# Kernel tuning notes

Hardware: AMD Instinct MI355X
Metric: run time of the kernel (lower is better)

Reference implementation:

```python
import jax, jax.numpy as jnp
import numpy as np

N_NODES = 50000
N_HEDGES = 5000
NNZ = 800000
IN_C = 128
D1 = 256
D2 = D1 // 4  # 64


def setup_inputs() -> dict:
    key = jax.random.key(0)
    ks = jax.random.split(key, 7)
    x = jax.random.normal(ks[0], (N_NODES, IN_C), dtype=jnp.float32)
    node_idx = jax.random.randint(ks[1], (NNZ,), 0, N_NODES, dtype=jnp.int32)
    hedge_idx = jax.random.randint(ks[2], (NNZ,), 0, N_HEDGES, dtype=jnp.int32)
    edge = jnp.stack([node_idx, hedge_idx], axis=0)  # [2, nnz]
    W1 = jax.random.normal(ks[3], (IN_C, D1), dtype=jnp.float32) / np.float32(np.sqrt(IN_C))
    b1 = jnp.zeros((D1,), dtype=jnp.float32)
    W2 = jax.random.normal(ks[4], (D1, D2), dtype=jnp.float32) / np.float32(np.sqrt(D1))
    b2 = jnp.zeros((D2,), dtype=jnp.float32)
    return {"x": x, "edge": edge, "W1": W1, "b1": b1, "W2": W2, "b2": b2}


def _hconv(x, W, b, node_idx, hedge_idx):
    # HypergraphConv (no attention, unit hyperedge weights):
    # out = D^{-1} H B^{-1} H^T (X W) + b
    xw = x @ W  # [N, F]
    ones = jnp.ones((node_idx.shape[0],), dtype=xw.dtype)
    deg = jax.ops.segment_sum(ones, node_idx, num_segments=N_NODES)      # D_i
    Dinv = jnp.where(deg > 0, 1.0 / deg, 0.0)
    cnt = jax.ops.segment_sum(ones, hedge_idx, num_segments=N_HEDGES)    # B_e
    Binv = jnp.where(cnt > 0, 1.0 / cnt, 0.0)
    # node -> hyperedge aggregation (gather + segment_sum), normalized by B^{-1}
    e = jax.ops.segment_sum(xw[node_idx], hedge_idx, num_segments=N_HEDGES) * Binv[:, None]
    # hyperedge -> node aggregation, normalized by D^{-1}
    out = jax.ops.segment_sum(e[hedge_idx], node_idx, num_segments=N_NODES) * Dinv[:, None]
    return out + b


def reference(x, edge, W1, b1, W2, b2):
    node_idx, hedge_idx = edge[0], edge[1]
    h = jax.nn.relu(_hconv(x, W1, b1, node_idx, hedge_idx))
    out = jax.nn.relu(_hconv(h, W2, b2, node_idx, hedge_idx))
    return out
```

## Files before the change

### kernel.cpp

```cpp
#include <hip/hip_runtime.h>

#define N_NODES 50000
#define N_HEDGES 5000
#define NNZ 800000
#define IN_C 128
#define D1 256
#define D2 64
#define SN 64
#define SH 256

#define HBK 20
#define NHB 250
#define HCAP 4096
#define NBK 100
#define NNB 500
#define NCAP 2048
#define BKT_BLOCKS ((NNZ + 2047) / 2048)

typedef unsigned int u32;
typedef unsigned short u16;
typedef __attribute__((ext_vector_type(8))) short short8;
typedef __attribute__((ext_vector_type(4))) float f32x4;

__device__ __forceinline__ float bf_lo(u32 u) { return __uint_as_float(u << 16); }
__device__ __forceinline__ float bf_hi(u32 u) { return __uint_as_float(u & 0xffff0000u); }
__device__ __forceinline__ u32 rne16(float f) {
    u32 u = __float_as_uint(f);
    return (u + 0x7fffu + ((u >> 16) & 1u)) >> 16;
}
__device__ __forceinline__ u32 pack2(float a, float b) {
    return rne16(a) | (rne16(b) << 16);
}
__device__ __forceinline__ void acc8(float* a, uint4 v) {
    a[0] += bf_lo(v.x); a[1] += bf_hi(v.x);
    a[2] += bf_lo(v.y); a[3] += bf_hi(v.y);
    a[4] += bf_lo(v.z); a[5] += bf_hi(v.z);
    a[6] += bf_lo(v.w); a[7] += bf_hi(v.w);
}

__global__ void cast_bucket(const float4* __restrict__ x, uint2* __restrict__ xb,
                            const float* __restrict__ W1, u16* __restrict__ w1hi,
                            u16* __restrict__ w1lo,
                            const float* __restrict__ W2, u16* __restrict__ w2hi,
                            u16* __restrict__ w2lo,
                            const int* __restrict__ nidx, const int* __restrict__ hidx,
                            int* __restrict__ gcur_h, int* __restrict__ gcur_n,
                            u32* __restrict__ pairs_h, u32* __restrict__ pairs_n) {
    __shared__ int hist_h[NHB], hist_n[NNB];
    __shared__ int base_h[NHB], base_n[NNB];
    int tid = threadIdx.x;
    int i = blockIdx.x * 256 + tid;
    float4 v = x[i];
    uint2 o;
    o.x = pack2(v.x, v.y);
    o.y = pack2(v.z, v.w);
    xb[i] = o;
    if (i < 32768) {
        int j = i & 7;
        int l = (i >> 3) & 63;
        int ct = (i >> 9) & 15;
        int kc = i >> 13;
        int k = kc * 32 + (l >> 4) * 8 + j;
        int n = ct * 16 + (l & 15);
        float w = W1[k * D1 + n];
        u32 h = rne16(w);
        w1hi[i] = (u16)h;
        w1lo[i] = (u16)rne16(w - bf_lo(h));
    } else if (i < 32768 + 16384) {
        int t = i - 32768;
        int j = t & 7;
        int l = (t >> 3) & 63;
        int nt = (t >> 9) & 3;
        int kc = t >> 11;
        int k = kc * 32 + (l >> 4) * 8 + j;
        int n = nt * 16 + (l & 15);
        float w = W2[k * D2 + n];
        u32 h = rne16(w);
        w2hi[t] = (u16)h;
        w2lo[t] = (u16)rne16(w - bf_lo(h));
    }
    if (blockIdx.x >= BKT_BLOCKS) return;
    for (int t = tid; t < NHB; t += 256) hist_h[t] = 0;
    for (int t = tid; t < NNB; t += 256) hist_n[t] = 0;
    __syncthreads();
    int e0 = blockIdx.x * 2048 + tid * 8;
    int ns[8], hs_[8];
#pragma unroll
    for (int k = 0; k < 8; k++) {
        int e = e0 + k;
        if (e < NNZ) {
            ns[k] = nidx[e];
            hs_[k] = hidx[e];
            atomicAdd(&hist_h[hs_[k] / HBK], 1);
            atomicAdd(&hist_n[ns[k] / NBK], 1);
        } else {
            ns[k] = -1;
        }
    }
    __syncthreads();
    if (tid < NHB) base_h[tid] = atomicAdd(&gcur_h[tid], hist_h[tid]);
    for (int t = tid; t < NNB; t += 256) base_n[t] = atomicAdd(&gcur_n[t], hist_n[t]);
    __syncthreads();
    for (int t = tid; t < NHB; t += 256) hist_h[t] = 0;
    for (int t = tid; t < NNB; t += 256) hist_n[t] = 0;
    __syncthreads();
#pragma unroll
    for (int k = 0; k < 8; k++) {
        if (ns[k] >= 0) {
            int n = ns[k], h = hs_[k];
            int bh = h / HBK, bn = n / NBK;
            int s1 = base_h[bh] + atomicAdd(&hist_h[bh], 1);
            if (s1 < HCAP) pairs_h[bh * HCAP + s1] = ((u32)h << 16) | (u32)n;
            int s2 = base_n[bn] + atomicAdd(&hist_n[bn], 1);
            if (s2 < NCAP) pairs_n[bn * NCAP + s2] = ((u32)n << 16) | (u32)h;
        }
    }
}

__global__ void build_adj(const u32* __restrict__ pairs_h, const int* __restrict__ gcur_h,
                          u16* __restrict__ adj_h, int* __restrict__ cur_h,
                          const u32* __restrict__ pairs_n, const int* __restrict__ gcur_n,
                          u16* __restrict__ adj_n, int* __restrict__ cur_n) {
    __shared__ u16 rows[NBK * SN];
    __shared__ int cnt[NBK];
    int tid = threadIdx.x;
    if (blockIdx.x < NHB) {
        int b = blockIdx.x;
        if (tid < HBK) cnt[tid] = 0;
        __syncthreads();
        int np = gcur_h[b];
        if (np > HCAP) np = HCAP;
        for (int t = tid; t < np; t += 256) {
            u32 p = pairs_h[b * HCAP + t];
            int hl = (int)(p >> 16) - b * HBK;
            int s = atomicAdd(&cnt[hl], 1);
            if (s < SH) rows[hl * SH + s] = (u16)(p & 0xffff);
        }
        __syncthreads();
        u32* dst = (u32*)(adj_h + b * HBK * SH);
        const u32* srcl = (const u32*)rows;
        for (int t = tid; t < HBK * SH / 2; t += 256) dst[t] = srcl[t];
        if (tid < HBK) cur_h[b * HBK + tid] = cnt[tid];
    } else {
        int b = blockIdx.x - NHB;
        if (tid < NBK) cnt[tid] = 0;
        __syncthreads();
        int np = gcur_n[b];
        if (np > NCAP) np = NCAP;
        for (int t = tid; t < np; t += 256) {
            u32 p = pairs_n[b * NCAP + t];
            int nl = (int)(p >> 16) - b * NBK;
            int s = atomicAdd(&cnt[nl], 1);
            if (s < SN) rows[nl * SN + s] = (u16)(p & 0xffff);
        }
        __syncthreads();
        u32* dst = (u32*)(adj_n + b * NBK * SN);
        const u32* srcl = (const u32*)rows;
        for (int t = tid; t < NBK * SN / 2; t += 256) dst[t] = srcl[t];
        if (tid < NBK) cur_n[b * NBK + tid] = cnt[tid];
    }
}

template <int F, int S, int SPLIT>
__global__ void gather_split(const uint4* __restrict__ src, const int* __restrict__ cur,
                             const u16* __restrict__ adj, uint4* __restrict__ dst,
                             int nrows) {
    constexpr int L = F / 8;
    constexpr int TR = L * SPLIT;
    constexpr int RB = 256 / TR;
    constexpr int CHUNK = S / SPLIT;
    __shared__ float part[RB][SPLIT][8];
    int tid = threadIdx.x;
    int rl = tid / TR;
    int seg = (tid % TR) / L;
    int c = tid % L;
    int row = blockIdx.x * RB + rl;
    bool valid = row < nrows;
    int len = valid ? cur[row] : 0;
    int lenc = (len < S) ? len : S;
    int js = seg * CHUNK;
    int je = (lenc < js + CHUNK) ? lenc : (js + CHUNK);
    float a0[8] = {0,0,0,0,0,0,0,0}, a1[8] = {0,0,0,0,0,0,0,0};
    float a2[8] = {0,0,0,0,0,0,0,0}, a3[8] = {0,0,0,0,0,0,0,0};
    if (valid) {
        const u16* arow = adj + row * S;
        int j = js;
        for (; j + 7 < je; j += 8) {
            uint4 aa = *(const uint4*)(arow + j);
            int i0 = aa.x & 0xffff, i1 = aa.x >> 16;
            int i2 = aa.y & 0xffff, i3 = aa.y >> 16;
            int i4 = aa.z & 0xffff, i5 = aa.z >> 16;
            int i6 = aa.w & 0xffff, i7 = aa.w >> 16;
            uint4 v0 = src[i0 * L + c];
            uint4 v1 = src[i1 * L + c];
            uint4 v2 = src[i2 * L + c];
            uint4 v3 = src[i3 * L + c];
            uint4 v4 = src[i4 * L + c];
            uint4 v5 = src[i5 * L + c];
            uint4 v6 = src[i6 * L + c];
            uint4 v7 = src[i7 * L + c];
            acc8(a0, v0); acc8(a1, v1); acc8(a2, v2); acc8(a3, v3);
            acc8(a0, v4); acc8(a1, v5); acc8(a2, v6); acc8(a3, v7);
        }
        for (; j < je; j++) {
            uint4 v = src[(int)arow[j] * L + c];
            acc8(a0, v);
        }
    }
    __shared__ float partf[256][8];
#pragma unroll
    for (int t = 0; t < 8; t++) partf[tid][t] = ((a0[t] + a1[t]) + (a2[t] + a3[t]));
    __syncthreads();
    if (seg == 0 && valid) {
        float r[8];
#pragma unroll
        for (int t = 0; t < 8; t++) r[t] = partf[tid][t];
#pragma unroll
        for (int s2 = 1; s2 < SPLIT; s2++) {
#pragma unroll
            for (int t = 0; t < 8; t++) r[t] += partf[tid + s2 * L][t];
        }
        float inv = (len > 0) ? 1.f / (float)len : 0.f;
        uint4 o;
        o.x = pack2(r[0] * inv, r[1] * inv);
        o.y = pack2(r[2] * inv, r[3] * inv);
        o.z = pack2(r[4] * inv, r[5] * inv);
        o.w = pack2(r[6] * inv, r[7] * inv);
        dst[row * L + c] = o;
    }
}

template <int F, int S, bool BIAS_RELU, bool DST_BF16>
__global__ void gatherb(const uint4* __restrict__ src, const int* __restrict__ cur,
                        const u16* __restrict__ adj, const float4* __restrict__ bias,
                        void* __restrict__ dst, int nrows) {
    constexpr int L = F / 8;
    int gid = blockIdx.x * 256 + threadIdx.x;
    int row = gid / L;
    if (row >= nrows) return;
    int c = gid - row * L;
    int len = cur[row];
    int lenc = (len < S) ? len : S;
    int s = row * S, e = s + lenc;
    float a0[8] = {0,0,0,0,0,0,0,0}, a1[8] = {0,0,0,0,0,0,0,0};
    float a2[8] = {0,0,0,0,0,0,0,0}, a3[8] = {0,0,0,0,0,0,0,0};
    int j = s;
    for (; j + 7 < e; j += 8) {
        uint4 aa = *(const uint4*)(adj + j);
        int i0 = aa.x & 0xffff, i1 = aa.x >> 16;
        int i2 = aa.y & 0xffff, i3 = aa.y >> 16;
        int i4 = aa.z & 0xffff, i5 = aa.z >> 16;
        int i6 = aa.w & 0xffff, i7 = aa.w >> 16;
        uint4 v0 = src[i0 * L + c];
        uint4 v1 = src[i1 * L + c];
        uint4 v2 = src[i2 * L + c];
        uint4 v3 = src[i3 * L + c];
        uint4 v4 = src[i4 * L + c];
        uint4 v5 = src[i5 * L + c];
        uint4 v6 = src[i6 * L + c];
        uint4 v7 = src[i7 * L + c];
        acc8(a0, v0); acc8(a1, v1); acc8(a2, v2); acc8(a3, v3);
        acc8(a0, v4); acc8(a1, v5); acc8(a2, v6); acc8(a3, v7);
    }
    for (; j < e; j++) {
        uint4 v = src[(int)adj[j] * L + c];
        acc8(a0, v);
    }
    float inv = (len > 0) ? 1.f / (float)len : 0.f;
    float r[8];
#pragma unroll
    for (int t = 0; t < 8; t++) r[t] = ((a0[t] + a1[t]) + (a2[t] + a3[t])) * inv;
    if (BIAS_RELU) {
        float4 b0 = bias[c * 2], b1v = bias[c * 2 + 1];
        r[0] = fmaxf(r[0] + b0.x, 0.f); r[1] = fmaxf(r[1] + b0.y, 0.f);
        r[2] = fmaxf(r[2] + b0.z, 0.f); r[3] = fmaxf(r[3] + b0.w, 0.f);
        r[4] = fmaxf(r[4] + b1v.x, 0.f); r[5] = fmaxf(r[5] + b1v.y, 0.f);
        r[6] = fmaxf(r[6] + b1v.z, 0.f); r[7] = fmaxf(r[7] + b1v.w, 0.f);
    }
    if (DST_BF16) {
        uint4 o;
        o.x = pack2(r[0], r[1]);
        o.y = pack2(r[2], r[3]);
        o.z = pack2(r[4], r[5]);
        o.w = pack2(r[6], r[7]);
        ((uint4*)dst)[row * L + c] = o;
    } else {
        float4* d = (float4*)dst;
        d[row * (F / 4) + c * 2]     = make_float4(r[0], r[1], r[2], r[3]);
        d[row * (F / 4) + c * 2 + 1] = make_float4(r[4], r[5], r[6], r[7]);
    }
}

#define SB_STRIDE 136
#define HSTRIDE 264
__global__ void gather_mlp(const uint4* __restrict__ aggxb4, const int* __restrict__ cur_n,
                           const u16* __restrict__ adj_n,
                           const short8* __restrict__ w1hi, const short8* __restrict__ w1lo,
                           const float* __restrict__ b1,
                           const short8* __restrict__ w2hi, const short8* __restrict__ w2lo,
                           u16* __restrict__ hw) {
    __shared__ u16 sbs[16 * SB_STRIDE];
    __shared__ u16 hs[16 * HSTRIDE];
    int tid = threadIdx.x;
    int node0 = blockIdx.x * 16;
    {
        int nl = tid >> 4;
        int c = tid & 15;
        int node = node0 + nl;
        int len = cur_n[node];
        int lenc = (len < SN) ? len : SN;
        const u16* adj = adj_n + node * SN;
        float a0[8] = {0,0,0,0,0,0,0,0}, a1[8] = {0,0,0,0,0,0,0,0};
        float a2[8] = {0,0,0,0,0,0,0,0}, a3[8] = {0,0,0,0,0,0,0,0};
        int j = 0;
        for (; j + 7 < lenc; j += 8) {
            uint4 aa = *(const uint4*)(adj + j);
            int i0 = aa.x & 0xffff, i1 = aa.x >> 16;
            int i2 = aa.y & 0xffff, i3 = aa.y >> 16;
            int i4 = aa.z & 0xffff, i5 = aa.z >> 16;
            int i6 = aa.w & 0xffff, i7 = aa.w >> 16;
            uint4 v0 = aggxb4[i0 * 16 + c];
            uint4 v1 = aggxb4[i1 * 16 + c];
            uint4 v2 = aggxb4[i2 * 16 + c];
            uint4 v3 = aggxb4[i3 * 16 + c];
            uint4 v4 = aggxb4[i4 * 16 + c];
            uint4 v5 = aggxb4[i5 * 16 + c];
            uint4 v6 = aggxb4[i6 * 16 + c];
            uint4 v7 = aggxb4[i7 * 16 + c];
            acc8(a0, v0); acc8(a1, v1); acc8(a2, v2); acc8(a3, v3);
            acc8(a0, v4); acc8(a1, v5); acc8(a2, v6); acc8(a3, v7);
        }
        for (; j < lenc; j++) {
            uint4 v = aggxb4[(int)adj[j] * 16 + c];
            acc8(a0, v);
        }
        float inv = (len > 0) ? 1.f / (float)len : 0.f;
        float r[8];
#pragma unroll
        for (int t = 0; t < 8; t++) r[t] = ((a0[t] + a1[t]) + (a2[t] + a3[t])) * inv;
        u32* dstl = (u32*)&sbs[nl * SB_STRIDE + c * 8];
        dstl[0] = pack2(r[0], r[1]);
        dstl[1] = pack2(r[2], r[3]);
        dstl[2] = pack2(r[4], r[5]);
        dstl[3] = pack2(r[6], r[7]);
    }
    __syncthreads();
    int wave = tid >> 6;
    int lane = tid & 63;
    int m = lane & 15;
    int q = lane >> 4;
    short8 a[4];
#pragma unroll
    for (int kc = 0; kc < 4; kc++)
        a[kc] = *(const short8*)&sbs[m * SB_STRIDE + kc * 32 + q * 8];
#pragma unroll
    for (int i = 0; i < 4; i++) {
        int ct = wave * 4 + i;
        f32x4 acc = {0.f, 0.f, 0.f, 0.f};
#pragma unroll
        for (int kc = 0; kc < 4; kc++) {
            acc = __builtin_amdgcn_mfma_f32_16x16x32_bf16(a[kc], w1hi[(kc * 16 + ct) * 64 + lane], acc, 0, 0, 0);
            acc = __builtin_amdgcn_mfma_f32_16x16x32_bf16(a[kc], w1lo[(kc * 16 + ct) * 64 + lane], acc, 0, 0, 0);
        }
        int col = ct * 16 + m;
        float bc = b1[col];
#pragma unroll
        for (int r = 0; r < 4; r++) {
            float h = fmaxf(acc[r] + bc, 0.f);
            hs[(q * 4 + r) * HSTRIDE + col] = (u16)rne16(h);
        }
    }
    __syncthreads();
    f32x4 acc = {0.f, 0.f, 0.f, 0.f};
#pragma unroll
    for (int kc = 0; kc < 8; kc++) {
        short8 ah = *(const short8*)&hs[m * HSTRIDE + kc * 32 + q * 8];
        acc = __builtin_amdgcn_mfma_f32_16x16x32_bf16(ah, w2hi[(kc * 4 + wave) * 64 + lane], acc, 0, 0, 0);
        acc = __builtin_amdgcn_mfma_f32_16x16x32_bf16(ah, w2lo[(kc * 4 + wave) * 64 + lane], acc, 0, 0, 0);
    }
#pragma unroll
    for (int r = 0; r < 4; r++) {
        hw[(node0 + q * 4 + r) * D2 + wave * 16 + m] = (u16)rne16(acc[r]);
    }
}

extern "C" void kernel_launch(void* const* d_in, const int* in_sizes, int n_in,
                              void* d_out, int out_size, void* d_ws, size_t ws_size,
                              hipStream_t stream) {
    const float* x  = (const float*)d_in[0];
    const int* edge = (const int*)d_in[1];
    const int* nidx = edge;
    const int* hidx = edge + NNZ;
    const float* W1 = (const float*)d_in[2];
    const float* b1 = (const float*)d_in[3];
    const float* W2 = (const float*)d_in[4];
    const float* b2 = (const float*)d_in[5];
    float* out = (float*)d_out;

    u16* xb     = (u16*)d_ws;
    u16* aggxb  = xb + N_NODES * IN_C;
    u16* hwb    = aggxb + N_HEDGES * IN_C;
    u16* e2b    = hwb + N_NODES * D2;
    u16* w1hi   = e2b + N_HEDGES * D2;
    u16* w1lo   = w1hi + 32768;
    u16* w2hi   = w1lo + 32768;
    u16* w2lo   = w2hi + 16384;
    u16* adj_n  = w2lo + 16384;
    u16* adj_h  = adj_n + N_NODES * SN;
    u32* pairs_h = (u32*)(adj_h + N_HEDGES * SH);
    u32* pairs_n = pairs_h + NHB * HCAP;
    int* cur_n  = (int*)(pairs_n + NNB * NCAP);
    int* cur_h  = cur_n + N_NODES;
    int* gcur_h = cur_h + N_HEDGES;
    int* gcur_n = gcur_h + 256;

    hipMemsetAsync(gcur_h, 0, (256 + 512) * sizeof(int), stream);

    cast_bucket<<<N_NODES * IN_C / 4 / 256, 256, 0, stream>>>(
        (const float4*)x, (uint2*)xb, W1, w1hi, w1lo, W2, w2hi, w2lo,
        nidx, hidx, gcur_h, gcur_n, pairs_h, pairs_n);

    build_adj<<<NHB + NNB, 256, 0, stream>>>(pairs_h, gcur_h, adj_h, cur_h,
                                             pairs_n, gcur_n, adj_n, cur_n);

    gather_split<IN_C, SH, 4><<<(N_HEDGES + 3) / 4, 256, 0, stream>>>(
        (const uint4*)xb, cur_h, adj_h, (uint4*)aggxb, N_HEDGES);

    gather_mlp<<<N_NODES / 16, 256, 0, stream>>>(
        (const uint4*)aggxb, cur_n, adj_n,
        (const short8*)w1hi, (const short8*)w1lo, b1,
        (const short8*)w2hi, (const short8*)w2lo, hwb);

    gather_split<D2, SH, 8><<<(N_HEDGES + 3) / 4, 256, 0, stream>>>(
        (const uint4*)hwb, cur_h, adj_h, (uint4*)e2b, N_HEDGES);
    gatherb<D2, SN, true, false><<<(N_NODES * (D2 / 8) + 255) / 256, 256, 0, stream>>>(
        (const uint4*)e2b, cur_n, adj_n, (const float4*)b2, out, N_NODES);
}
```

Measured before the change: 221.7 us.

## Process 64 nodes per block in gather_mlp to reuse weight fragments across M tiles

The fused gather+MLP kernel now handles 64 nodes per block instead of 16. Each thread gathers four node rows, and each wave's MFMA loops run over four M tiles so every loaded W1/W2 fragment is reused four times. Bias is folded into the accumulator initialisation, launch bounds are set, and partial tail blocks are guarded. The larger register and LDS footprint may lower occupancy and the number of blocks in flight during the latency-bound gather phase.

Result: no change. 225.4 us (+1.7%).

```diff
diff --git a/kernel.cpp b/kernel.cpp
--- a/kernel.cpp
+++ b/kernel.cpp
@@ -169,7 +169,6 @@
     constexpr int TR = L * SPLIT;
     constexpr int RB = 256 / TR;
     constexpr int CHUNK = S / SPLIT;
-    __shared__ float part[RB][SPLIT][8];
     int tid = threadIdx.x;
     int rl = tid / TR;
     int seg = (tid % TR) / L;
@@ -293,95 +292,133 @@
 
 #define SB_STRIDE 136
 #define HSTRIDE 264
-__global__ void gather_mlp(const uint4* __restrict__ aggxb4, const int* __restrict__ cur_n,
-                           const u16* __restrict__ adj_n,
-                           const short8* __restrict__ w1hi, const short8* __restrict__ w1lo,
-                           const float* __restrict__ b1,
-                           const short8* __restrict__ w2hi, const short8* __restrict__ w2lo,
-                           u16* __restrict__ hw) {
-    __shared__ u16 sbs[16 * SB_STRIDE];
-    __shared__ u16 hs[16 * HSTRIDE];
+__global__ __launch_bounds__(256, 3)
+void gather_mlp(const uint4* __restrict__ aggxb4, const int* __restrict__ cur_n,
+                const u16* __restrict__ adj_n,
+                const short8* __restrict__ w1hi, const short8* __restrict__ w1lo,
+                const float* __restrict__ b1,
+                const short8* __restrict__ w2hi, const short8* __restrict__ w2lo,
+                u16* __restrict__ hw) {
+    __shared__ u16 sbs[64 * SB_STRIDE];
+    __shared__ u16 hs[64 * HSTRIDE];
     int tid = threadIdx.x;
-    int node0 = blockIdx.x * 16;
+    int node0 = blockIdx.x * 64;
     {
-        int nl = tid >> 4;
         int c = tid & 15;
-        int node = node0 + nl;
-        int len = cur_n[node];
-        int lenc = (len < SN) ? len : SN;
-        const u16* adj = adj_n + node * SN;
-        float a0[8] = {0,0,0,0,0,0,0,0}, a1[8] = {0,0,0,0,0,0,0,0};
-        float a2[8] = {0,0,0,0,0,0,0,0}, a3[8] = {0,0,0,0,0,0,0,0};
-        int j = 0;
-        for (; j + 7 < lenc; j += 8) {
-            uint4 aa = *(const uint4*)(adj + j);
-            int i0 = aa.x & 0xffff, i1 = aa.x >> 16;
-            int i2 = aa.y & 0xffff, i3 = aa.y >> 16;
-            int i4 = aa.z & 0xffff, i5 = aa.z >> 16;
-            int i6 = aa.w & 0xffff, i7 = aa.w >> 16;
-            uint4 v0 = aggxb4[i0 * 16 + c];
-            uint4 v1 = aggxb4[i1 * 16 + c];
-            uint4 v2 = aggxb4[i2 * 16 + c];
-            uint4 v3 = aggxb4[i3 * 16 + c];
-            uint4 v4 = aggxb4[i4 * 16 + c];
-            uint4 v5 = aggxb4[i5 * 16 + c];
-            uint4 v6 = aggxb4[i6 * 16 + c];
-            uint4 v7 = aggxb4[i7 * 16 + c];
-            acc8(a0, v0); acc8(a1, v1); acc8(a2, v2); acc8(a3, v3);
-            acc8(a0, v4); acc8(a1, v5); acc8(a2, v6); acc8(a3, v7);
-        }
-        for (; j < lenc; j++) {
-            uint4 v = aggxb4[(int)adj[j] * 16 + c];
-            acc8(a0, v);
-        }
-        float inv = (len > 0) ? 1.f / (float)len : 0.f;
-        float r[8];
-#pragma unroll
-        for (int t = 0; t < 8; t++) r[t] = ((a0[t] + a1[t]) + (a2[t] + a3[t])) * inv;
-        u32* dstl = (u32*)&sbs[nl * SB_STRIDE + c * 8];
-        dstl[0] = pack2(r[0], r[1]);
-        dstl[1] = pack2(r[2], r[3]);
-        dstl[2] = pack2(r[4], r[5]);
-        dstl[3] = pack2(r[6], r[7]);
+        int nlb = tid >> 4;
+#pragma unroll
+        for (int rep = 0; rep < 4; rep++) {
+            int nl = nlb + rep * 16;
+            int node = node0 + nl;
+            int len = (node < N_NODES) ? cur_n[node] : 0;
+            int lenc = (len < SN) ? len : SN;
+            const u16* adj = adj_n + node * SN;
+            float a0[8] = {0,0,0,0,0,0,0,0}, a1[8] = {0,0,0,0,0,0,0,0};
+            float a2[8] = {0,0,0,0,0,0,0,0}, a3[8] = {0,0,0,0,0,0,0,0};
+            int j = 0;
+            for (; j + 7 < lenc; j += 8) {
+                uint4 aa = *(const uint4*)(adj + j);
+                int i0 = aa.x & 0xffff, i1 = aa.x >> 16;
+                int i2 = aa.y & 0xffff, i3 = aa.y >> 16;
+                int i4 = aa.z & 0xffff, i5 = aa.z >> 16;
+                int i6 = aa.w & 0xffff, i7 = aa.w >> 16;
+                uint4 v0 = aggxb4[i0 * 16 + c];
+                uint4 v1 = aggxb4[i1 * 16 + c];
+                uint4 v2 = aggxb4[i2 * 16 + c];
+                uint4 v3 = aggxb4[i3 * 16 + c];
+                uint4 v4 = aggxb4[i4 * 16 + c];
+                uint4 v5 = aggxb4[i5 * 16 + c];
+                uint4 v6 = aggxb4[i6 * 16 + c];
+                uint4 v7 = aggxb4[i7 * 16 + c];
+                acc8(a0, v0); acc8(a1, v1); acc8(a2, v2); acc8(a3, v3);
+                acc8(a0, v4); acc8(a1, v5); acc8(a2, v6); acc8(a3, v7);
+            }
+            for (; j < lenc; j++) {
+                uint4 v = aggxb4[(int)adj[j] * 16 + c];
+                acc8(a0, v);
+            }
+            float inv = (len > 0) ? 1.f / (float)len : 0.f;
+            float r[8];
+#pragma unroll
+            for (int t = 0; t < 8; t++) r[t] = ((a0[t] + a1[t]) + (a2[t] + a3[t])) * inv;
+            u32* dstl = (u32*)&sbs[nl * SB_STRIDE + c * 8];
+            dstl[0] = pack2(r[0], r[1]);
+            dstl[1] = pack2(r[2], r[3]);
+            dstl[2] = pack2(r[4], r[5]);
+            dstl[3] = pack2(r[6], r[7]);
+        }
     }
     __syncthreads();
     int wave = tid >> 6;
     int lane = tid & 63;
     int m = lane & 15;
     int q = lane >> 4;
-    short8 a[4];
-#pragma unroll
-    for (int kc = 0; kc < 4; kc++)
-        a[kc] = *(const short8*)&sbs[m * SB_STRIDE + kc * 32 + q * 8];
+    float bc[4];
+#pragma unroll
+    for (int i = 0; i < 4; i++) bc[i] = b1[(wave * 4 + i) * 16 + m];
+    f32x4 acc[4][4];
+#pragma unroll
+    for (int i = 0; i < 4; i++)
+#pragma unroll
+        for (int mt = 0; mt < 4; mt++)
+            acc[i][mt] = (f32x4){bc[i], bc[i], bc[i], bc[i]};
+#pragma unroll
+    for (int kc = 0; kc < 4; kc++) {
+        short8 am[4];
+#pragma unroll
+        for (int mt = 0; mt < 4; mt++)
+            am[mt] = *(const short8*)&sbs[(mt * 16 + m) * SB_STRIDE + kc * 32 + q * 8];
+        short8 whi[4], wlo[4];
+#pragma unroll
+        for (int i = 0; i < 4; i++) {
+            whi[i] = w1hi[(kc * 16 + wave * 4 + i) * 64 + lane];
+            wlo[i] = w1lo[(kc * 16 + wave * 4 + i) * 64 + lane];
+        }
+#pragma unroll
+        for (int i = 0; i < 4; i++)
+#pragma unroll
+            for (int mt = 0; mt < 4; mt++) {
+                acc[i][mt] = __builtin_amdgcn_mfma_f32_16x16x32_bf16(am[mt], whi[i], acc[i][mt], 0, 0, 0);
+                acc[i][mt] = __builtin_amdgcn_mfma_f32_16x16x32_bf16(am[mt], wlo[i], acc[i][mt], 0, 0, 0);
+            }
+    }
 #pragma unroll
     for (int i = 0; i < 4; i++) {
-        int ct = wave * 4 + i;
-        f32x4 acc = {0.f, 0.f, 0.f, 0.f};
-#pragma unroll
-        for (int kc = 0; kc < 4; kc++) {
-            acc = __builtin_amdgcn_mfma_f32_16x16x32_bf16(a[kc], w1hi[(kc * 16 + ct) * 64 + lane], acc, 0, 0, 0);
-            acc = __builtin_amdgcn_mfma_f32_16x16x32_bf16(a[kc], w1lo[(kc * 16 + ct) * 64 + lane], acc, 0, 0, 0);
-        }
-        int col = ct * 16 + m;
-        float bc = b1[col];
+        int col = (wave * 4 + i) * 16 + m;
+#pragma unroll
+        for (int mt = 0; mt < 4; mt++)
+#pragma unroll
+            for (int r = 0; r < 4; r++) {
+                float h = fmaxf(acc[i][mt][r], 0.f);
+                hs[(mt * 16 + q * 4 + r) * HSTRIDE + col] = (u16)rne16(h);
+            }
+    }
+    __syncthreads();
+    f32x4 acc2[4];
+#pragma unroll
+    for (int mt = 0; mt < 4; mt++) acc2[mt] = (f32x4){0.f, 0.f, 0.f, 0.f};
+#pragma unroll
+    for (int kc = 0; kc < 8; kc++) {
+        short8 ah[4];
+#pragma unroll
+        for (int mt = 0; mt < 4; mt++)
+            ah[mt] = *(const short8*)&hs[(mt * 16 + m) * HSTRIDE + kc * 32 + q * 8];
+        short8 whi = w2hi[(kc * 4 + wave) * 64 + lane];
+        short8 wlo = w2lo[(kc * 4 + wave) * 64 + lane];
+#pragma unroll
+        for (int mt = 0; mt < 4; mt++) {
+            acc2[mt] = __builtin_amdgcn_mfma_f32_16x16x32_bf16(ah[mt], whi, acc2[mt], 0, 0, 0);
+            acc2[mt] = __builtin_amdgcn_mfma_f32_16x16x32_bf16(ah[mt], wlo, acc2[mt], 0, 0, 0);
+        }
+    }
+#pragma unroll
+    for (int mt = 0; mt < 4; mt++)
 #pragma unroll
         for (int r = 0; r < 4; r++) {
-            float h = fmaxf(acc[r] + bc, 0.f);
-            hs[(q * 4 + r) * HSTRIDE + col] = (u16)rne16(h);
-        }
-    }
-    __syncthreads();
-    f32x4 acc = {0.f, 0.f, 0.f, 0.f};
-#pragma unroll
-    for (int kc = 0; kc < 8; kc++) {
-        short8 ah = *(const short8*)&hs[m * HSTRIDE + kc * 32 + q * 8];
-        acc = __builtin_amdgcn_mfma_f32_16x16x32_bf16(ah, w2hi[(kc * 4 + wave) * 64 + lane], acc, 0, 0, 0);
-        acc = __builtin_amdgcn_mfma_f32_16x16x32_bf16(ah, w2lo[(kc * 4 + wave) * 64 + lane], acc, 0, 0, 0);
-    }
-#pragma unroll
-    for (int r = 0; r < 4; r++) {
-        hw[(node0 + q * 4 + r) * D2 + wave * 16 + m] = (u16)rne16(acc[r]);
-    }
+            int row = node0 + mt * 16 + q * 4 + r;
+            if (row < N_NODES)
+                hw[row * D2 + wave * 16 + m] = (u16)rne16(acc2[mt][r]);
+        }
 }
 
 extern "C" void kernel_launch(void* const* d_in, const int* in_sizes, int n_in,
@@ -426,7 +463,7 @@
     gather_split<IN_C, SH, 4><<<(N_HEDGES + 3) / 4, 256, 0, stream>>>(
         (const uint4*)xb, cur_h, adj_h, (uint4*)aggxb, N_HEDGES);
 
-    gather_mlp<<<N_NODES / 16, 256, 0, stream>>>(
+    gather_mlp<<<(N_NODES + 63) / 64, 256, 0, stream>>>(
         (const uint4*)aggxb, cur_n, adj_n,
         (const short8*)w1hi, (const short8*)w1lo, b1,
         (const short8*)w2hi, (const short8*)w2lo, hwb);
```
